# Kernel optimization log

Measured on AMD Instinct MI355X. Metric: run time of the kernel, lower is better.

Reference implementation:

```python
import jax, jax.numpy as jnp
import numpy as np

N = 50000
E = 800000
IN = 128
HID = 32
HEADS = 4
OUT = 32
NEG_SLOPE = 0.2  # PyG GATConv default


def setup_inputs() -> dict:
    key = jax.random.key(0)
    ks = jax.random.split(key, 16)
    s = lambda k, sh: jax.random.normal(k, sh, jnp.float32) * 0.05
    inp = {}
    inp["x"] = jax.random.normal(ks[0], (N, IN), jnp.float32)
    inp["edge_idx"] = jax.random.randint(ks[1], (2, E), 0, N)
    inp["edge_attr"] = jax.random.normal(ks[2], (E, 1), jnp.float32)
    inp["lin1_w"] = s(ks[3], (IN, HEADS * HID))
    inp["att1_src"] = s(ks[4], (HEADS, HID))
    inp["att1_dst"] = s(ks[5], (HEADS, HID))
    inp["lin1_edge_w"] = s(ks[6], (1, HEADS * HID))
    inp["att1_edge"] = s(ks[7], (HEADS, HID))
    inp["bias1"] = jnp.zeros((HEADS * HID,), jnp.float32)
    inp["lin2_w"] = s(ks[8], (HEADS * HID, OUT))
    inp["att2_src"] = s(ks[9], (1, OUT))
    inp["att2_dst"] = s(ks[10], (1, OUT))
    inp["lin2_edge_w"] = s(ks[11], (1, OUT))
    inp["att2_edge"] = s(ks[12], (1, OUT))
    inp["bias2"] = jnp.zeros((OUT,), jnp.float32)
    return inp


def _gat_conv(x, src, dst, eattr, lin_w, a_src, a_dst, lin_e, a_e, bias, heads, ch, concat):
    """PyG GATConv (eval mode): gather -> leaky_relu logits -> segment softmax over dst -> scatter-sum."""
    n = x.shape[0]
    xl = (x @ lin_w).reshape(n, heads, ch)                      # [N,H,C]
    alpha = ((xl * a_src).sum(-1)[src]                          # [Etot,H]
             + (xl * a_dst).sum(-1)[dst]
             + ((eattr @ lin_e).reshape(-1, heads, ch) * a_e).sum(-1))
    alpha = jax.nn.leaky_relu(alpha, NEG_SLOPE)
    amax = jax.ops.segment_max(alpha, dst, num_segments=n)      # every node has a self-loop
    ex = jnp.exp(alpha - amax[dst])
    den = jax.ops.segment_sum(ex, dst, num_segments=n)
    w = ex / den[dst]                                           # [Etot,H]
    out = jax.ops.segment_sum(w[:, :, None] * xl[src], dst, num_segments=n)  # [N,H,C]
    out = out.reshape(n, heads * ch) if concat else out.mean(axis=1)
    return out + bias


def reference(x, edge_idx, edge_attr,
              lin1_w, att1_src, att1_dst, lin1_edge_w, att1_edge, bias1,
              lin2_w, att2_src, att2_dst, lin2_edge_w, att2_edge, bias2):
    n = x.shape[0]
    # add_self_loops=True with edge_attr fill_value='mean' (PyG default when edge_dim is set)
    loops = jnp.arange(n)
    src = jnp.concatenate([edge_idx[0], loops])
    dst = jnp.concatenate([edge_idx[1], loops])
    ea = jnp.concatenate(
        [edge_attr, jnp.broadcast_to(edge_attr.mean(0, keepdims=True), (n, edge_attr.shape[1]))], 0)
    h = jax.nn.elu(_gat_conv(x, src, dst, ea, lin1_w, att1_src, att1_dst,
                             lin1_edge_w, att1_edge, bias1, HEADS, HID, True))
    # F.dropout with training=False -> identity (eval mode)
    return _gat_conv(h, src, dst, ea, lin2_w, att2_src, att2_dst,
                     lin2_edge_w, att2_edge, bias2, 1, OUT, True)
```

## Files before the change

### kernel.cpp

```cpp
#include <hip/hip_runtime.h>
#include <hip/hip_fp16.h>
#include <math.h>

#define NN   50000
#define EE   800000
#define ETOT 850000
#define NEG  0.2f
#define SCAN_BLOCKS ((NN + 255) / 256)

#define O_DEG    0
#define O_EASUM  50000
#define ZERO_ELEMS 50004
#define O_COEF   50004
#define O_ROWPTR 50012
#define O_CURSOR 100016
#define O_BLKSUM 150016
#define O_SLOT   150528
#define O_ASRC1  1850528
#define O_ADST1  2050528
#define O_XLH    2250528
#define O_OUT1   5450528
#define O_HLH    11850528
#define O_ASRC2  12650528
#define O_ADST2  12700528
#define WS_ELEMS 12750528

__global__ void k_ea_count(const float* __restrict__ ea, const int* __restrict__ ei,
                           const float* __restrict__ lew1, const float* __restrict__ ae1,
                           const float* __restrict__ lew2, const float* __restrict__ ae2,
                           float* __restrict__ easum, int* __restrict__ deg,
                           float* __restrict__ coef) {
  if (blockIdx.x == 0 && threadIdx.x < 128) {
    int t = threadIdx.x;
    float p = lew1[t] * ae1[t];
    #pragma unroll
    for (int o = 16; o > 0; o >>= 1) p += __shfl_down(p, o, 32);
    if ((t & 31) == 0) coef[t >> 5] = p;
    if (t < 32) {
      float q = lew2[t] * ae2[t];
      #pragma unroll
      for (int o = 16; o > 0; o >>= 1) q += __shfl_down(q, o, 32);
      if (t == 0) coef[4] = q;
    }
  }
  __shared__ float red[4];
  float s = 0.f;
  int stride = gridDim.x * blockDim.x;
  for (int i = blockIdx.x * blockDim.x + threadIdx.x; i < EE; i += stride) {
    s += ea[i];
    atomicAdd(deg + ei[EE + i], 1);
  }
  #pragma unroll
  for (int o = 32; o > 0; o >>= 1) s += __shfl_down(s, o, 64);
  if ((threadIdx.x & 63) == 0) red[threadIdx.x >> 6] = s;
  __syncthreads();
  if (threadIdx.x == 0) atomicAdd(easum, red[0] + red[1] + red[2] + red[3]);
}

__device__ __forceinline__ int wave_incl_scan(int v, int lane) {
  #pragma unroll
  for (int o = 1; o < 64; o <<= 1) {
    int u = __shfl_up(v, o, 64);
    if (lane >= o) v += u;
  }
  return v;
}

__global__ __launch_bounds__(256) void k_scan_blk(const int* __restrict__ deg,
                                                  int* __restrict__ rowptr,
                                                  int* __restrict__ blksum) {
  __shared__ int wsum[4];
  const int t = threadIdx.x;
  const int i = blockIdx.x * 256 + t;
  const int lane = t & 63, wv = t >> 6;
  int v = (i < NN) ? (deg[i] + 1) : 0;
  int incl = wave_incl_scan(v, lane);
  if (lane == 63) wsum[wv] = incl;
  __syncthreads();
  int off = 0;
  #pragma unroll
  for (int k = 0; k < 4; ++k) if (k < wv) off += wsum[k];
  incl += off;
  if (i < NN) rowptr[i] = incl - v;
  if (t == 255) blksum[blockIdx.x] = incl;
}

__global__ __launch_bounds__(256) void k_scan_add(int* __restrict__ rowptr,
                                                  int* __restrict__ cursor,
                                                  const int* __restrict__ blksum) {
  __shared__ int wsum[4];
  const int t = threadIdx.x;
  int v = (t < SCAN_BLOCKS && t < (int)blockIdx.x) ? blksum[t] : 0;
  #pragma unroll
  for (int o = 32; o > 0; o >>= 1) v += __shfl_down(v, o, 64);
  if ((t & 63) == 0) wsum[t >> 6] = v;
  __syncthreads();
  const int off = wsum[0] + wsum[1] + wsum[2] + wsum[3];
  const int i = blockIdx.x * 256 + t;
  if (i < NN) {
    int r = rowptr[i] + off;
    rowptr[i] = r;
    cursor[i] = r;
  }
  if (i == 0) rowptr[NN] = ETOT;
}

#define FILL_CHUNK  2048
#define FILL_NCHUNK ((ETOT + FILL_CHUNK - 1) / FILL_CHUNK)
#define NODES_PER_GRP (NN / 8)
__global__ __launch_bounds__(256) void k_fill(
    const int* __restrict__ ei, const float* __restrict__ eattr,
    const float* __restrict__ easum, int* __restrict__ cursor,
    unsigned* __restrict__ slot) {
  const int g    = blockIdx.x & 7;
  const int c    = blockIdx.x >> 3;
  const int dlo  = g * NODES_PER_GRP;
  const int dhi  = dlo + NODES_PER_GRP;
  const int base = c * FILL_CHUNK;
  #pragma unroll
  for (int it = 0; it < FILL_CHUNK / 256; ++it) {
    const int e = base + it * 256 + threadIdx.x;
    if (e < ETOT) {
      int d = (e < EE) ? ei[EE + e] : (e - EE);
      if (d >= dlo && d < dhi) {
        int s; float ea;
        if (e < EE) { s = ei[e]; ea = eattr[e]; }
        else { s = d; ea = easum[0] * (1.f / EE); }
        int sl = atomicAdd(cursor + d, 1);
        unsigned hb = (unsigned)__half_as_ushort(__float2half_rn(ea));
        slot[sl] = (unsigned)s | (hb << 16);
      }
    }
  }
}

#define GEMM_STEP(WB, K, XS) {                                              \
    const float4* Wr = (const float4*)((WB) + (size_t)(K));                 \
    _Pragma("unroll")                                                       \
    for (int j4 = 0; j4 < 8; ++j4) {                                        \
      float4 wv = Wr[j4];                                                   \
      acc[j4 * 4 + 0] += (XS) * wv.x;                                       \
      acc[j4 * 4 + 1] += (XS) * wv.y;                                       \
      acc[j4 * 4 + 2] += (XS) * wv.z;                                       \
      acc[j4 * 4 + 3] += (XS) * wv.w;                                       \
    } }

#define L1_NB ((NN + 63) / 64)
__global__ __launch_bounds__(256) void k_lin1(
    const float* __restrict__ x, const float* __restrict__ W,
    const float* __restrict__ att_src, const float* __restrict__ att_dst,
    __half* __restrict__ xlh, float* __restrict__ asrc, float* __restrict__ adst) {
  const int h   = __builtin_amdgcn_readfirstlane(threadIdx.x >> 6);
  const int n   = blockIdx.x * 64 + (threadIdx.x & 63);
  const int nc  = n < NN ? n : NN - 1;
  const float4* xr = (const float4*)(x + (size_t)nc * 128);
  const float*  Wh = W + h * 32;
  float acc[32];
  #pragma unroll
  for (int j = 0; j < 32; ++j) acc[j] = 0.f;
  float4 xv = xr[0];
  for (int kt = 0; kt < 32; ++kt) {
    float4 cur = xv;
    if (kt < 31) xv = xr[kt + 1];
    GEMM_STEP(Wh, (kt * 4 + 0) * 128, cur.x);
    GEMM_STEP(Wh, (kt * 4 + 1) * 128, cur.y);
    GEMM_STEP(Wh, (kt * 4 + 2) * 128, cur.z);
    GEMM_STEP(Wh, (kt * 4 + 3) * 128, cur.w);
  }
  if (n < NN) {
    __align__(16) __half hbuf[32];
    #pragma unroll
    for (int j = 0; j < 32; ++j) hbuf[j] = __float2half_rn(acc[j]);
    float4* dst = (float4*)(xlh + (size_t)n * 128 + h * 32);
    #pragma unroll
    for (int i = 0; i < 4; ++i) dst[i] = ((const float4*)hbuf)[i];
    float ss = 0.f, sd = 0.f;
    #pragma unroll
    for (int j = 0; j < 32; ++j) {
      ss += acc[j] * att_src[h * 32 + j];
      sd += acc[j] * att_dst[h * 32 + j];
    }
    asrc[n * 4 + h] = ss;
    adst[n * 4 + h] = sd;
  }
}

__global__ __launch_bounds__(256) void k_agg1(
    const int* __restrict__ rowptr, const unsigned* __restrict__ slot,
    const float* __restrict__ asrc, const float* __restrict__ adst,
    const float* __restrict__ coef, const __half* __restrict__ xlh,
    float* __restrict__ out1) {
  int n = blockIdx.x * 8 + (threadIdx.x >> 5);
  if (n >= NN) return;
  int l = threadIdx.x & 31;
  int c4 = l << 2;
  int h = l >> 3;
  float cf = coef[h];
  float ad = adst[(size_t)n * 4 + h];
  int r0 = rowptr[n], r1 = rowptr[n + 1];
  float a0 = 0.f, a1 = 0.f, a2 = 0.f, a3 = 0.f, den = 0.f;
  for (int j = r0; j < r1; j += 4) {
    unsigned sd[4]; float asv[4]; uint2 raw[4];
    #pragma unroll
    for (int k = 0; k < 4; ++k) {
      int jj = (j + k < r1) ? (j + k) : (r1 - 1);
      sd[k] = slot[jj];
    }
    #pragma unroll
    for (int k = 0; k < 4; ++k) {
      int sn = (int)(sd[k] & 0xFFFFu);
      asv[k] = asrc[(size_t)sn * 4 + h];
      raw[k] = *(const uint2*)(xlh + (size_t)sn * 128 + c4);
    }
    #pragma unroll
    for (int k = 0; k < 4; ++k) {
      float eav = __half2float(__ushort_as_half((unsigned short)(sd[k] >> 16)));
      float alpha = asv[k] + ad + eav * cf;
      alpha = alpha > 0.f ? alpha : NEG * alpha;
      float ex = (j + k < r1) ? __expf(alpha) : 0.f;
      __half2 p0, p1;
      *(unsigned int*)&p0 = raw[k].x;
      *(unsigned int*)&p1 = raw[k].y;
      float2 f0 = __half22float2(p0), f1 = __half22float2(p1);
      a0 += ex * f0.x;
      a1 += ex * f0.y;
      a2 += ex * f1.x;
      a3 += ex * f1.y;
      den += ex;
    }
  }
  float inv = 1.f / den;
  *(float4*)(out1 + (size_t)n * 128 + c4) = make_float4(a0 * inv, a1 * inv, a2 * inv, a3 * inv);
}

__global__ __launch_bounds__(256) void k_lin2(
    const float* __restrict__ out1, const float* __restrict__ bias1,
    const float* __restrict__ W2,
    const float* __restrict__ as2w, const float* __restrict__ ad2w,
    __half* __restrict__ hlh, float* __restrict__ asrc2, float* __restrict__ adst2) {
  const int n  = blockIdx.x * 256 + threadIdx.x;
  const int nc = n < NN ? n : NN - 1;
  const float4* xr = (const float4*)(out1 + (size_t)nc * 128);
  const float4* br = (const float4*)bias1;
  float acc[32];
  #pragma unroll
  for (int j = 0; j < 32; ++j) acc[j] = 0.f;
  float4 xv = xr[0];
  for (int kt = 0; kt < 32; ++kt) {
    float4 cur = xv;
    if (kt < 31) xv = xr[kt + 1];
    float4 b = br[kt];
    cur.x += b.x; cur.y += b.y; cur.z += b.z; cur.w += b.w;
    cur.x = cur.x > 0.f ? cur.x : (expf(cur.x) - 1.f);
    cur.y = cur.y > 0.f ? cur.y : (expf(cur.y) - 1.f);
    cur.z = cur.z > 0.f ? cur.z : (expf(cur.z) - 1.f);
    cur.w = cur.w > 0.f ? cur.w : (expf(cur.w) - 1.f);
    GEMM_STEP(W2, (kt * 4 + 0) * 32, cur.x);
    GEMM_STEP(W2, (kt * 4 + 1) * 32, cur.y);
    GEMM_STEP(W2, (kt * 4 + 2) * 32, cur.z);
    GEMM_STEP(W2, (kt * 4 + 3) * 32, cur.w);
  }
  if (n < NN) {
    __align__(16) __half hbuf[32];
    #pragma unroll
    for (int j = 0; j < 32; ++j) hbuf[j] = __float2half_rn(acc[j]);
    float4* dst = (float4*)(hlh + (size_t)n * 32);
    #pragma unroll
    for (int i = 0; i < 4; ++i) dst[i] = ((const float4*)hbuf)[i];
    float ps = 0.f, pd = 0.f;
    #pragma unroll
    for (int j = 0; j < 32; ++j) {
      ps += acc[j] * as2w[j];
      pd += acc[j] * ad2w[j];
    }
    asrc2[n] = ps;
    adst2[n] = pd;
  }
}

__global__ __launch_bounds__(256) void k_agg2(
    const int* __restrict__ rowptr, const unsigned* __restrict__ slot,
    const float* __restrict__ asrc2, const float* __restrict__ adst2,
    const float* __restrict__ coef, const __half* __restrict__ hlh,
    const float* __restrict__ bias2, float* __restrict__ out) {
  int n = blockIdx.x * 32 + (threadIdx.x >> 3);
  if (n >= NN) return;
  int c4 = (threadIdx.x & 7) << 2;
  float cf = coef[4];
  float ad = adst2[n];
  int r0 = rowptr[n], r1 = rowptr[n + 1];
  float a0 = 0.f, a1 = 0.f, a2 = 0.f, a3 = 0.f, den = 0.f;
  for (int j = r0; j < r1; j += 4) {
    unsigned sd[4]; float asv[4]; uint2 raw[4];
    #pragma unroll
    for (int k = 0; k < 4; ++k) {
      int jj = (j + k < r1) ? (j + k) : (r1 - 1);
      sd[k] = slot[jj];
    }
    #pragma unroll
    for (int k = 0; k < 4; ++k) {
      int sn = (int)(sd[k] & 0xFFFFu);
      asv[k] = asrc2[sn];
      raw[k] = *(const uint2*)(hlh + (size_t)sn * 32 + c4);
    }
    #pragma unroll
    for (int k = 0; k < 4; ++k) {
      float eav = __half2float(__ushort_as_half((unsigned short)(sd[k] >> 16)));
      float alpha = asv[k] + ad + eav * cf;
      alpha = alpha > 0.f ? alpha : NEG * alpha;
      float ex = (j + k < r1) ? __expf(alpha) : 0.f;
      __half2 p0, p1;
      *(unsigned int*)&p0 = raw[k].x;
      *(unsigned int*)&p1 = raw[k].y;
      float2 f0 = __half22float2(p0), f1 = __half22float2(p1);
      a0 += ex * f0.x;
      a1 += ex * f0.y;
      a2 += ex * f1.x;
      a3 += ex * f1.y;
      den += ex;
    }
  }
  float inv = 1.f / den;
  float4 b = *(const float4*)(bias2 + c4);
  *(float4*)(out + (size_t)n * 32 + c4) =
      make_float4(a0 * inv + b.x, a1 * inv + b.y, a2 * inv + b.z, a3 * inv + b.w);
}

extern "C" void kernel_launch(void* const* d_in, const int* in_sizes, int n_in,
                              void* d_out, int out_size, void* d_ws, size_t ws_size,
                              hipStream_t stream) {
  const float* x        = (const float*)d_in[0];
  const int*   ei       = (const int*)d_in[1];
  const float* eattr    = (const float*)d_in[2];
  const float* lin1_w   = (const float*)d_in[3];
  const float* att1_src = (const float*)d_in[4];
  const float* att1_dst = (const float*)d_in[5];
  const float* lin1_ew  = (const float*)d_in[6];
  const float* att1_e   = (const float*)d_in[7];
  const float* bias1    = (const float*)d_in[8];
  const float* lin2_w   = (const float*)d_in[9];
  const float* att2_src = (const float*)d_in[10];
  const float* att2_dst = (const float*)d_in[11];
  const float* lin2_ew  = (const float*)d_in[12];
  const float* att2_e   = (const float*)d_in[13];
  const float* bias2    = (const float*)d_in[14];
  float* out = (float*)d_out;
  float* ws  = (float*)d_ws;
  int*   wsi = (int*)d_ws;

  int*      deg     = wsi + O_DEG;
  float*    easum   = ws + O_EASUM;
  float*    coef    = ws + O_COEF;
  int*      rowptr  = wsi + O_ROWPTR;
  int*      cursor  = wsi + O_CURSOR;
  int*      blksum  = wsi + O_BLKSUM;
  unsigned* slot    = (unsigned*)(ws + O_SLOT);
  float*    asrc1   = ws + O_ASRC1;
  float*    adst1   = ws + O_ADST1;
  __half*   xlh     = (__half*)(ws + O_XLH);
  float*    out1    = ws + O_OUT1;
  __half*   hlh     = (__half*)(ws + O_HLH);
  float*    asrc2   = ws + O_ASRC2;
  float*    adst2   = ws + O_ADST2;

  hipMemsetAsync(ws, 0, (size_t)ZERO_ELEMS * sizeof(float), stream);

  k_ea_count<<<256, 256, 0, stream>>>(eattr, ei, lin1_ew, att1_e, lin2_ew, att2_e,
                                      easum, deg, coef);

  k_scan_blk<<<SCAN_BLOCKS, 256, 0, stream>>>(deg, rowptr, blksum);
  k_scan_add<<<SCAN_BLOCKS, 256, 0, stream>>>(rowptr, cursor, blksum);
  k_fill<<<FILL_NCHUNK * 8, 256, 0, stream>>>(ei, eattr, easum, cursor, slot);

  k_lin1<<<L1_NB, 256, 0, stream>>>(x, lin1_w, att1_src, att1_dst, xlh, asrc1, adst1);
  k_agg1<<<(NN + 7) / 8, 256, 0, stream>>>(rowptr, slot, asrc1, adst1, coef, xlh, out1);

  k_lin2<<<(NN + 255) / 256, 256, 0, stream>>>(out1, bias1, lin2_w, att2_src, att2_dst, hlh, asrc2, adst2);
  k_agg2<<<(NN + 31) / 32, 256, 0, stream>>>(rowptr, slot, asrc2, adst2, coef, hlh, bias2, out);
}
```

Before: 292.9 us.

## Fuse layer-1 aggregation with bias, ELU and layer-2 linear projection

The first-layer aggregation kernel now applies bias1 and ELU in registers and stages each node's 128-wide row in shared memory. The 32 lanes of that node's group then compute the 32 outputs of the second linear layer, write the half-precision features, and reduce the layer-2 attention scalars with shuffles. This removes the fp32 out1 round trip through global memory and one kernel launch. In exchange, the shared-memory handoff relies on wavefront lockstep with no barrier, and the matmul is now done per node rather than per thread-row.

```diff
diff --git a/kernel.cpp b/kernel.cpp
--- a/kernel.cpp
+++ b/kernel.cpp
@@ -19,11 +19,12 @@
 #define O_ASRC1  1850528
 #define O_ADST1  2050528
 #define O_XLH    2250528
-#define O_OUT1   5450528
 #define O_HLH    11850528
 #define O_ASRC2  12650528
 #define O_ADST2  12700528
 #define WS_ELEMS 12750528
+
+#define NODES_PER_GRP (NN / 8)
 
 __global__ void k_ea_count(const float* __restrict__ ea, const int* __restrict__ ei,
                            const float* __restrict__ lew1, const float* __restrict__ ae1,
@@ -107,7 +108,6 @@
 
 #define FILL_CHUNK  2048
 #define FILL_NCHUNK ((ETOT + FILL_CHUNK - 1) / FILL_CHUNK)
-#define NODES_PER_GRP (NN / 8)
 __global__ __launch_bounds__(256) void k_fill(
     const int* __restrict__ ei, const float* __restrict__ eattr,
     const float* __restrict__ easum, int* __restrict__ cursor,
@@ -185,12 +185,16 @@
   }
 }
 
-__global__ __launch_bounds__(256) void k_agg1(
+__global__ __launch_bounds__(256) void k_agg1l2(
     const int* __restrict__ rowptr, const unsigned* __restrict__ slot,
     const float* __restrict__ asrc, const float* __restrict__ adst,
     const float* __restrict__ coef, const __half* __restrict__ xlh,
-    float* __restrict__ out1) {
-  int n = blockIdx.x * 8 + (threadIdx.x >> 5);
+    const float* __restrict__ bias1, const float* __restrict__ W2,
+    const float* __restrict__ as2w, const float* __restrict__ ad2w,
+    __half* __restrict__ hlh, float* __restrict__ asrc2, float* __restrict__ adst2) {
+  __shared__ float rowbuf[8][132];
+  int nl = threadIdx.x >> 5;
+  int n = blockIdx.x * 8 + nl;
   if (n >= NN) return;
   int l = threadIdx.x & 31;
   int c4 = l << 2;
@@ -230,49 +234,31 @@
     }
   }
   float inv = 1.f / den;
-  *(float4*)(out1 + (size_t)n * 128 + c4) = make_float4(a0 * inv, a1 * inv, a2 * inv, a3 * inv);
-}
-
-__global__ __launch_bounds__(256) void k_lin2(
-    const float* __restrict__ out1, const float* __restrict__ bias1,
-    const float* __restrict__ W2,
-    const float* __restrict__ as2w, const float* __restrict__ ad2w,
-    __half* __restrict__ hlh, float* __restrict__ asrc2, float* __restrict__ adst2) {
-  const int n  = blockIdx.x * 256 + threadIdx.x;
-  const int nc = n < NN ? n : NN - 1;
-  const float4* xr = (const float4*)(out1 + (size_t)nc * 128);
-  const float4* br = (const float4*)bias1;
-  float acc[32];
-  #pragma unroll
-  for (int j = 0; j < 32; ++j) acc[j] = 0.f;
-  float4 xv = xr[0];
-  for (int kt = 0; kt < 32; ++kt) {
-    float4 cur = xv;
-    if (kt < 31) xv = xr[kt + 1];
-    float4 b = br[kt];
-    cur.x += b.x; cur.y += b.y; cur.z += b.z; cur.w += b.w;
-    cur.x = cur.x > 0.f ? cur.x : (expf(cur.x) - 1.f);
-    cur.y = cur.y > 0.f ? cur.y : (expf(cur.y) - 1.f);
-    cur.z = cur.z > 0.f ? cur.z : (expf(cur.z) - 1.f);
-    cur.w = cur.w > 0.f ? cur.w : (expf(cur.w) - 1.f);
-    GEMM_STEP(W2, (kt * 4 + 0) * 32, cur.x);
-    GEMM_STEP(W2, (kt * 4 + 1) * 32, cur.y);
-    GEMM_STEP(W2, (kt * 4 + 2) * 32, cur.z);
-    GEMM_STEP(W2, (kt * 4 + 3) * 32, cur.w);
-  }
-  if (n < NN) {
-    __align__(16) __half hbuf[32];
-    #pragma unroll
-    for (int j = 0; j < 32; ++j) hbuf[j] = __float2half_rn(acc[j]);
-    float4* dst = (float4*)(hlh + (size_t)n * 32);
-    #pragma unroll
-    for (int i = 0; i < 4; ++i) dst[i] = ((const float4*)hbuf)[i];
-    float ps = 0.f, pd = 0.f;
-    #pragma unroll
-    for (int j = 0; j < 32; ++j) {
-      ps += acc[j] * as2w[j];
-      pd += acc[j] * ad2w[j];
-    }
+  float4 b = *(const float4*)(bias1 + c4);
+  float v0 = a0 * inv + b.x, v1 = a1 * inv + b.y;
+  float v2 = a2 * inv + b.z, v3 = a3 * inv + b.w;
+  v0 = v0 > 0.f ? v0 : (expf(v0) - 1.f);
+  v1 = v1 > 0.f ? v1 : (expf(v1) - 1.f);
+  v2 = v2 > 0.f ? v2 : (expf(v2) - 1.f);
+  v3 = v3 > 0.f ? v3 : (expf(v3) - 1.f);
+  rowbuf[nl][c4 + 0] = v0;
+  rowbuf[nl][c4 + 1] = v1;
+  rowbuf[nl][c4 + 2] = v2;
+  rowbuf[nl][c4 + 3] = v3;
+  const int col = l;
+  const float* rw = rowbuf[nl];
+  float hsum = 0.f;
+  #pragma unroll 4
+  for (int k = 0; k < 128; ++k) hsum += rw[k] * W2[k * 32 + col];
+  hlh[(size_t)n * 32 + col] = __float2half_rn(hsum);
+  float ps = hsum * as2w[col];
+  float pd = hsum * ad2w[col];
+  #pragma unroll
+  for (int o = 1; o < 32; o <<= 1) {
+    ps += __shfl_xor(ps, o, 64);
+    pd += __shfl_xor(pd, o, 64);
+  }
+  if (l == 0) {
     asrc2[n] = ps;
     adst2[n] = pd;
   }
@@ -358,7 +344,6 @@
   float*    asrc1   = ws + O_ASRC1;
   float*    adst1   = ws + O_ADST1;
   __half*   xlh     = (__half*)(ws + O_XLH);
-  float*    out1    = ws + O_OUT1;
   __half*   hlh     = (__half*)(ws + O_HLH);
   float*    asrc2   = ws + O_ASRC2;
   float*    adst2   = ws + O_ADST2;
@@ -373,8 +358,10 @@
   k_fill<<<FILL_NCHUNK * 8, 256, 0, stream>>>(ei, eattr, easum, cursor, slot);
 
   k_lin1<<<L1_NB, 256, 0, stream>>>(x, lin1_w, att1_src, att1_dst, xlh, asrc1, adst1);
-  k_agg1<<<(NN + 7) / 8, 256, 0, stream>>>(rowptr, slot, asrc1, adst1, coef, xlh, out1);
-
-  k_lin2<<<(NN + 255) / 256, 256, 0, stream>>>(out1, bias1, lin2_w, att2_src, att2_dst, hlh, asrc2, adst2);
+
+  k_agg1l2<<<(NN + 7) / 8, 256, 0, stream>>>(rowptr, slot, asrc1, adst1, coef, xlh,
+                                             bias1, lin2_w, att2_src, att2_dst,
+                                             hlh, asrc2, adst2);
+
   k_agg2<<<(NN + 31) / 32, 256, 0, stream>>>(rowptr, slot, asrc2, adst2, coef, hlh, bias2, out);
 }
```

Measured after the change: 283.4 us. 1.03x faster.
